# Optimization experiments

Hardware: AMD Instinct MI355X
Metric: run time of the kernel (lower is better)

Reference implementation:

```python
import jax, jax.numpy as jnp
import numpy as np

N_EMBD = 2048
N_HEAD = 8          # config.n_head // 2
HEAD_DIM = 256      # n_embd // (n_head // 2)
HALF = HEAD_DIM // 2
LAMBDA_INIT = 0.8
RMS_EPS = 1.1920929e-07  # torch float32 finfo eps (F.rms_norm default)


def _rms_norm(x):
    # F.rms_norm with no weight: x / sqrt(mean(x^2) + eps)
    return x * jax.lax.rsqrt(jnp.mean(x * x, axis=-1, keepdims=True) + RMS_EPS)


def setup_inputs() -> dict:
    key = jax.random.key(0)
    ks = jax.random.split(key, 10)
    B, T, C = 2, 2048, N_EMBD
    x = jax.random.normal(ks[0], (B, T, C), dtype=jnp.float32)
    wq = jax.random.normal(ks[1], (C, C), dtype=jnp.float32) * 0.02
    wk = jax.random.normal(ks[2], (C, C), dtype=jnp.float32) * 0.02
    wv = jax.random.normal(ks[3], (C, C), dtype=jnp.float32) * 0.02
    wo = jax.random.normal(ks[4], (C, C), dtype=jnp.float32) * 0.02
    lq1 = jax.random.normal(ks[5], (HEAD_DIM,), dtype=jnp.float32) * 0.1
    lk1 = jax.random.normal(ks[6], (HEAD_DIM,), dtype=jnp.float32) * 0.1
    lq2 = jax.random.normal(ks[7], (HEAD_DIM,), dtype=jnp.float32) * 0.1
    lk2 = jax.random.normal(ks[8], (HEAD_DIM,), dtype=jnp.float32) * 0.1
    return {"x": x, "wq": wq, "wk": wk, "wv": wv, "wo": wo,
            "lq1": lq1, "lk1": lk1, "lq2": lq2, "lk2": lk2}


def _causal_attn(q, k, v, mask):
    # q,k: [B,H,T,half], v: [B,H,T,HEAD_DIM]
    scale = 1.0 / jnp.sqrt(jnp.asarray(q.shape[-1], q.dtype))
    scores = jnp.einsum('bhqd,bhkd->bhqk', q, k) * scale
    scores = jnp.where(mask, scores, -jnp.inf)
    attn = jax.nn.softmax(scores, axis=-1)
    return jnp.einsum('bhqk,bhkd->bhqd', attn, v)


def reference(x, wq, wk, wv, wo, lq1, lk1, lq2, lk2):
    B, T, C = x.shape
    lambda_1 = jnp.exp(jnp.sum(lq1 * lk1))
    lambda_2 = jnp.exp(jnp.sum(lq2 * lk2))
    lambda_full = lambda_1 - lambda_2 + LAMBDA_INIT

    q = (x @ wq.T).reshape(B, T, N_HEAD, 2, HALF).transpose(0, 2, 1, 3, 4)  # [B,H,T,2,half]
    k = (x @ wk.T).reshape(B, T, N_HEAD, 2, HALF).transpose(0, 2, 1, 3, 4)
    v = (x @ wv.T).reshape(B, T, N_HEAD, HEAD_DIM).transpose(0, 2, 1, 3)    # [B,H,T,hd]

    q1 = _rms_norm(q[..., 0, :]); q2 = _rms_norm(q[..., 1, :])
    k1 = _rms_norm(k[..., 0, :]); k2 = _rms_norm(k[..., 1, :])

    mask = jnp.tril(jnp.ones((T, T), dtype=bool))
    y1 = _causal_attn(q1, k1, v, mask)
    y2 = _causal_attn(q2, k2, v, mask)
    y = y1 - lambda_full * y2                                               # [B,H,T,hd]

    y = y.transpose(0, 2, 1, 3).reshape(B, T, C)
    return (y @ wo.T) * (1.0 - LAMBDA_INIT)
```

## Files before the change

### kernel.cpp

```cpp
#include <hip/hip_runtime.h>
#include <stdint.h>


typedef __bf16 bf16;
typedef bf16 bf16x8 __attribute__((ext_vector_type(8)));
typedef bf16 bf16x4 __attribute__((ext_vector_type(4)));
typedef bf16 bf16x2 __attribute__((ext_vector_type(2)));
typedef float f32x4 __attribute__((ext_vector_type(4)));

typedef void __attribute__((address_space(1)))* gas_t;
typedef void __attribute__((address_space(3)))* las_t;

__device__ __forceinline__ void gload16(const void* g, void* l) {
  __builtin_amdgcn_global_load_lds((gas_t)(uintptr_t)g, (las_t)(uint32_t)(uintptr_t)l, 16, 0, 0);
}

__device__ __forceinline__ f32x4 mfma16x16(bf16x8 a, bf16x8 b, f32x4 c) {
  return __builtin_amdgcn_mfma_f32_16x16x32_bf16(a, b, c, 0, 0, 0);
}

__global__ __launch_bounds__(256) void cast_f32_bf16(const float* __restrict__ in,
                                                     bf16* __restrict__ out, int n4) {
  int i = blockIdx.x * 256 + threadIdx.x;
  if (i >= n4) return;
  float4 v = ((const float4*)in)[i];
  bf16x4 o;
  o[0] = (bf16)v.x; o[1] = (bf16)v.y; o[2] = (bf16)v.z; o[3] = (bf16)v.w;
  ((bf16x4*)out)[i] = o;
}

__global__ __launch_bounds__(256) void cast4_w(const float* __restrict__ a, const float* __restrict__ b,
                                               const float* __restrict__ c, const float* __restrict__ d,
                                               bf16* __restrict__ oa, bf16* __restrict__ ob,
                                               bf16* __restrict__ oc, bf16* __restrict__ od) {
  int w = blockIdx.y;
  const float* in = (w == 0) ? a : (w == 1) ? b : (w == 2) ? c : d;
  bf16* out = (w == 0) ? oa : (w == 1) ? ob : (w == 2) ? oc : od;
  int i = blockIdx.x * 256 + threadIdx.x;
  float4 v = ((const float4*)in)[i];
  bf16x4 o;
  o[0] = (bf16)v.x; o[1] = (bf16)v.y; o[2] = (bf16)v.z; o[3] = (bf16)v.w;
  ((bf16x4*)out)[i] = o;
}

__global__ void lambda_kernel(const float* __restrict__ lq1, const float* __restrict__ lk1,
                              const float* __restrict__ lq2, const float* __restrict__ lk2,
                              float* __restrict__ out) {
  __shared__ float red[8];
  int tid = threadIdx.x;
  float a = lq1[tid] * lk1[tid];
  float b = lq2[tid] * lk2[tid];
#pragma unroll
  for (int m = 32; m >= 1; m >>= 1) {
    a += __shfl_xor(a, m, 64);
    b += __shfl_xor(b, m, 64);
  }
  if ((tid & 63) == 0) { red[tid >> 6] = a; red[4 + (tid >> 6)] = b; }
  __syncthreads();
  if (tid == 0) {
    float s1 = red[0] + red[1] + red[2] + red[3];
    float s2 = red[4] + red[5] + red[6] + red[7];
    out[0] = expf(s1) - expf(s2) + 0.8f;
  }
}

__global__ __launch_bounds__(512, 2) void gemm_qkv8(const bf16* __restrict__ A,
                                                    const bf16* __restrict__ Bq,
                                                    const bf16* __restrict__ Bk,
                                                    const bf16* __restrict__ Bv,
                                                    bf16* __restrict__ Cq, bf16* __restrict__ Ck,
                                                    bf16* __restrict__ Cv) {
  __shared__ char lds[98304];
  const int K = 2048, nt = 64;

  int p = blockIdx.y * gridDim.x + blockIdx.x;
  int lid = (p & 7) * 48 + (p >> 3);
  const int bm = (lid / 24) * 256;
  const int bnG = (lid % 24) * 256;
  const int z = bnG >> 11;
  const int bn = bnG & 2047;
  const bf16* B = (z == 0) ? Bq : ((z == 1) ? Bk : Bv);

  const int tid = threadIdx.x;
  const int wid = tid >> 6, lane = tid & 63;
  const int l15 = lane & 15, lhi = lane >> 4;
  const int wm = wid >> 2, wn = wid & 3;

  const bf16* aS0 = A + (size_t)(bm + wid * 16 + l15) * K + lhi * 8;
  const bf16* bS0 = B + (size_t)(bn + wid * 16 + l15) * K + lhi * 8;

  auto stA = [&](int t, int pb) {
    char* d = lds + pb * 32768 + wid * 1024;
    const bf16* s = aS0 + t * 32;
    gload16(s, d);
    gload16(s + (size_t)128 * K, d + 8192);
  };
  auto stB = [&](int t, int pb) {
    char* d = lds + pb * 32768 + 16384 + wid * 1024;
    const bf16* s = bS0 + t * 32;
    gload16(s, d);
    gload16(s + (size_t)128 * K, d + 8192);
  };

  const f32x4 fz = {0.f, 0.f, 0.f, 0.f};
  f32x4 acc[8][4];
#pragma unroll
  for (int m = 0; m < 8; ++m)
#pragma unroll
    for (int n = 0; n < 4; ++n) acc[m][n] = fz;

  stA(0, 0); stB(0, 0);
  stA(1, 1); stB(1, 1);
  asm volatile("s_waitcnt vmcnt(4)" ::: "memory");
  __builtin_amdgcn_s_barrier();

  int cur = 0;
  for (int t = 0; t < nt; ++t) {
    const char* ab = lds + cur * 32768;
    const char* bb = ab + 16384;
    int nx2 = cur + 2; if (nx2 >= 3) nx2 -= 3;
    bf16x8 a[8], b0, b1;

#pragma unroll
    for (int m = 0; m < 8; ++m) a[m] = *(const bf16x8*)(ab + (wm * 8 + m) * 1024 + lane * 16);
    b0 = *(const bf16x8*)(bb + (wn * 4 + 0) * 1024 + lane * 16);
    b1 = *(const bf16x8*)(bb + (wn * 4 + 1) * 1024 + lane * 16);
    if (t + 2 < nt) stA(t + 2, nx2);
    __builtin_amdgcn_s_barrier();
    __builtin_amdgcn_s_setprio(1);
#pragma unroll
    for (int m = 0; m < 8; ++m) {
      acc[m][0] = mfma16x16(a[m], b0, acc[m][0]);
      acc[m][1] = mfma16x16(a[m], b1, acc[m][1]);
    }
    __builtin_amdgcn_s_setprio(0);
    __builtin_amdgcn_s_barrier();

    b0 = *(const bf16x8*)(bb + (wn * 4 + 2) * 1024 + lane * 16);
    b1 = *(const bf16x8*)(bb + (wn * 4 + 3) * 1024 + lane * 16);
    if (t + 2 < nt) stB(t + 2, nx2);
    __builtin_amdgcn_s_barrier();
    __builtin_amdgcn_s_setprio(1);
#pragma unroll
    for (int m = 0; m < 8; ++m) {
      acc[m][2] = mfma16x16(a[m], b0, acc[m][2]);
      acc[m][3] = mfma16x16(a[m], b1, acc[m][3]);
    }
    __builtin_amdgcn_s_setprio(0);
    if (t + 2 < nt) {
      asm volatile("s_waitcnt vmcnt(4)" ::: "memory");
    } else {
      asm volatile("s_waitcnt vmcnt(0)" ::: "memory");
    }
    __builtin_amdgcn_s_barrier();

    cur = (cur == 2) ? 0 : cur + 1;
  }

  if (z == 2) {
#pragma unroll
    for (int m = 0; m < 8; ++m)
#pragma unroll
      for (int n = 0; n < 4; ++n)
#pragma unroll
        for (int r = 0; r < 4; ++r) {
          int row = bm + wm * 128 + m * 16 + lhi * 4 + r;
          int col = bn + wn * 64 + n * 16 + l15;
          int bb3 = row >> 11, tt = row & 2047;
          Cv[(size_t)bb3 * 2048 * 2048 + (size_t)col * 2048 + tt] = (bf16)acc[m][n][r];
        }
    return;
  }
  float* ldsf = (float*)lds;
#pragma unroll
  for (int m = 0; m < 8; ++m)
#pragma unroll
    for (int r = 0; r < 4; ++r) {
      float s = acc[m][0][r] * acc[m][0][r] + acc[m][1][r] * acc[m][1][r] +
                acc[m][2][r] * acc[m][2][r] + acc[m][3][r] * acc[m][3][r];
      s += __shfl_xor(s, 1, 64);
      s += __shfl_xor(s, 2, 64);
      s += __shfl_xor(s, 4, 64);
      s += __shfl_xor(s, 8, 64);
      if (l15 == 0) ldsf[(wm * 128 + m * 16 + lhi * 4 + r) * 4 + wn] = s;
    }
  __syncthreads();
  const float osc = (z == 0) ? 0.08838834764831845f : 1.0f;
  bf16* C = (z == 0) ? Cq : Ck;
#pragma unroll
  for (int m = 0; m < 8; ++m) {
#pragma unroll
    for (int r = 0; r < 4; ++r) {
      int rl = wm * 128 + m * 16 + lhi * 4 + r;
      float tot = ldsf[rl * 4 + (wn & 2)] + ldsf[rl * 4 + (wn & 2) + 1];
      float sc = rsqrtf(tot * (1.0f / 128.0f) + 1.1920929e-07f) * osc;
#pragma unroll
      for (int n = 0; n < 4; ++n) {
        int col = bn + wn * 64 + n * 16 + l15;
        C[(size_t)(bm + rl) * 2048 + col] = (bf16)(acc[m][n][r] * sc);
      }
    }
  }
}

__global__ __launch_bounds__(256, 2) void gemm_out(const bf16* __restrict__ A, const bf16* __restrict__ B,
                                                   float* __restrict__ Cf) {
  __shared__ char lds[73728];
  const int K = 2048, nt = 64;

  int p = blockIdx.y * gridDim.x + blockIdx.x;
  int lid = (p & 7) * 32 + (p >> 3);
  const int bm = (lid / 16) * 256;
  const int bn = (lid % 16) * 128;

  const int tid = threadIdx.x;
  const int wid = tid >> 6, lane = tid & 63;
  const int l15 = lane & 15, lhi = lane >> 4;
  const int wm = wid >> 1, wn = wid & 1;

  const bf16* aB = A + (size_t)(bm + l15) * K + lhi * 8;
  const bf16* bB = B + (size_t)(bn + l15) * K + lhi * 8;

  auto stage = [&](int t, int pb) {
    char* base = lds + pb * 24576;
    const int k0 = t * 32;
    gload16(aB + (size_t)((0 + wid) * 16) * K + k0, base + wid * 1024);
    gload16(aB + (size_t)((4 + wid) * 16) * K + k0, base + 4096 + wid * 1024);
    gload16(aB + (size_t)((8 + wid) * 16) * K + k0, base + 8192 + wid * 1024);
    gload16(aB + (size_t)((12 + wid) * 16) * K + k0, base + 12288 + wid * 1024);
    gload16(bB + (size_t)((0 + wid) * 16) * K + k0, base + 16384 + wid * 1024);
    gload16(bB + (size_t)((4 + wid) * 16) * K + k0, base + 20480 + wid * 1024);
  };

  const f32x4 fz = {0.f, 0.f, 0.f, 0.f};
  f32x4 acc[8][4];
#pragma unroll
  for (int m = 0; m < 8; ++m)
#pragma unroll
    for (int n = 0; n < 4; ++n) acc[m][n] = fz;

  stage(0, 0);
  stage(1, 1);
  asm volatile("s_waitcnt vmcnt(6)" ::: "memory");
  __builtin_amdgcn_s_barrier();

  for (int t = 0; t < nt; ++t) {
    const char* ab = lds + (t % 3) * 24576;
    if (t + 2 < nt) stage(t + 2, (t + 2) % 3);
    bf16x8 a[8], b[4];
#pragma unroll
    for (int m = 0; m < 8; ++m)
      a[m] = *(const bf16x8*)(ab + (wm * 8 + m) * 1024 + lane * 16);
#pragma unroll
    for (int n = 0; n < 4; ++n)
      b[n] = *(const bf16x8*)(ab + 16384 + (wn * 4 + n) * 1024 + lane * 16);
    __builtin_amdgcn_s_setprio(1);
#pragma unroll
    for (int m = 0; m < 8; ++m)
#pragma unroll
      for (int n = 0; n < 4; ++n) acc[m][n] = mfma16x16(a[m], b[n], acc[m][n]);
    __builtin_amdgcn_s_setprio(0);
    if (t + 2 < nt) {
      asm volatile("s_waitcnt vmcnt(6)" ::: "memory");
    } else {
      asm volatile("s_waitcnt vmcnt(0)" ::: "memory");
    }
    __builtin_amdgcn_s_barrier();
  }

#pragma unroll
  for (int m = 0; m < 8; ++m)
#pragma unroll
    for (int n = 0; n < 4; ++n)
#pragma unroll
      for (int r = 0; r < 4; ++r) {
        int row = bm + wm * 128 + m * 16 + lhi * 4 + r;
        int col = bn + wn * 64 + n * 16 + l15;
        Cf[(size_t)row * 2048 + col] = acc[m][n][r] * 0.2f;
      }
}

__global__ __launch_bounds__(256) void attn_kernel(const bf16* __restrict__ qb, const bf16* __restrict__ kb,
                                                   const bf16* __restrict__ vtb, bf16* __restrict__ yb,
                                                   const float* __restrict__ lamp) {
  __shared__ char lds[73728];
  const int tid = threadIdx.x;
  const int wid = tid >> 6, lane = tid & 63;
  const int l15 = lane & 15, lhi = lane >> 4;
  char* p1l = lds + 65536 + wid * 2048;
  char* p2l = p1l + 1024;

  const int p = blockIdx.x;
  const int bh = p & 15;
  const int qt = (p < 256) ? (31 - (p >> 4)) : ((p - 256) >> 4);
  const int b = bh >> 3, h = bh & 7;
  const int qr0 = qt * 64 + wid * 16;
  const float lam = lamp[0];

  const bf16* qrow = qb + (size_t)(b * 2048 + qr0 + l15) * 2048 + h * 256 + lhi * 8;
  bf16x8 q1f[4], q2f[4];
#pragma unroll
  for (int s = 0; s < 4; ++s) {
    q1f[s] = *(const bf16x8*)(qrow + s * 32);
    q2f[s] = *(const bf16x8*)(qrow + 128 + s * 32);
  }

  const f32x4 fz = {0.f, 0.f, 0.f, 0.f};
  f32x4 y1[16], y2[16];
#pragma unroll
  for (int f = 0; f < 16; ++f) { y1[f] = fz; y2[f] = fz; }
  float l1[4] = {0.f, 0.f, 0.f, 0.f}, l2[4] = {0.f, 0.f, 0.f, 0.f};

  const int nkt = 2 * qt + 2;
  const bf16* kbase = kb + (size_t)(b * 2048) * 2048 + h * 256;
  const bf16* vbase = vtb + (size_t)b * 2048 * 2048 + (size_t)(h * 256) * 2048;

  auto stageK = [&](int kt2, int pp) {
    const int t0 = kt2 * 32;
    char* kd = lds + pp * 16384 + wid * 1024;
    const bf16* sp = kbase + (size_t)(t0 + l15) * 2048 + wid * 32 + lhi * 8;
    gload16(sp, kd);
    gload16(sp + 16 * 2048, kd + 4096);
    gload16(sp + 128, kd + 8192);
    gload16(sp + 16 * 2048 + 128, kd + 12288);
  };
  auto stageVT = [&](int kt2, int pp) {
    const int t0 = kt2 * 32;
    char* vd = lds + 32768 + pp * 16384;
    const bf16* vp = vbase + (size_t)(wid * 16 + l15) * 2048 + t0 + lhi * 8;
#pragma unroll
    for (int i = 0; i < 4; ++i)
      gload16(vp + (size_t)i * 64 * 2048, vd + (i * 4 + wid) * 1024);
  };

  stageK(0, 0);
  stageVT(0, 0);
  __syncthreads();

  for (int kt = 0; kt < nkt; ++kt) {
    const int cur = kt & 1;
    const int t0 = kt * 32;
    const bool active = (t0 <= qr0 + 15);
    if (kt + 1 < nkt) {
      stageK(kt + 1, cur ^ 1);
      stageVT(kt + 1, cur ^ 1);
    }
    if (active) {
      const char* kc = lds + cur * 16384;
      const char* vc = lds + 32768 + cur * 16384;
      f32x4 s1g[2], s2g[2];
      __builtin_amdgcn_s_setprio(1);
#pragma unroll
      for (int g = 0; g < 2; ++g) {
        f32x4 a1 = fz, a2 = fz;
#pragma unroll
        for (int s = 0; s < 4; ++s) {
          a1 = mfma16x16(q1f[s], *(const bf16x8*)(kc + ((g * 4 + s) * 64 + lane) * 16), a1);
          a2 = mfma16x16(q2f[s], *(const bf16x8*)(kc + 8192 + ((g * 4 + s) * 64 + lane) * 16), a2);
        }
        s1g[g] = a1;
        s2g[g] = a2;
      }
      __builtin_amdgcn_s_setprio(0);
      if (t0 + 31 > qr0) {
#pragma unroll
        for (int g = 0; g < 2; ++g) {
          int col = t0 + g * 16 + l15;
#pragma unroll
          for (int r = 0; r < 4; ++r) {
            int row = qr0 + lhi * 4 + r;
            if (col > row) { s1g[g][r] = -1e30f; s2g[g][r] = -1e30f; }
          }
        }
      }
#pragma unroll
      for (int g = 0; g < 2; ++g) {
#pragma unroll
        for (int r = 0; r < 4; ++r) {
          float p1 = __expf(s1g[g][r] - 12.0f);
          float p2 = __expf(s2g[g][r] - 12.0f);
          l1[r] += p1;
          l2[r] += p2;
          int off = ((lhi * 4 + r) * 32 + g * 16 + l15) * 2;
          *(bf16*)(p1l + off) = (bf16)p1;
          *(bf16*)(p2l + off) = (bf16)p2;
        }
      }
      bf16x8 pa1 = *(const bf16x8*)(p1l + (l15 * 32 + lhi * 8) * 2);
      bf16x8 pa2 = *(const bf16x8*)(p2l + (l15 * 32 + lhi * 8) * 2);
      __builtin_amdgcn_s_setprio(1);
#pragma unroll
      for (int f = 0; f < 16; ++f) {
        bf16x8 vf = *(const bf16x8*)(vc + (f * 64 + lane) * 16);
        y1[f] = mfma16x16(pa1, vf, y1[f]);
        y2[f] = mfma16x16(pa2, vf, y2[f]);
      }
      __builtin_amdgcn_s_setprio(0);
    }
    __syncthreads();
  }

#pragma unroll
  for (int r = 0; r < 4; ++r) {
    float s1 = l1[r], s2 = l2[r];
#pragma unroll
    for (int m = 1; m <= 8; m <<= 1) {
      s1 += __shfl_xor(s1, m, 64);
      s2 += __shfl_xor(s2, m, 64);
    }
    float inv1 = 1.f / s1;
    float inv2 = lam / s2;
    int row = qr0 + lhi * 4 + r;
    bf16* orow = yb + (size_t)(b * 2048 + row) * 2048 + h * 256 + l15;
#pragma unroll
    for (int f = 0; f < 16; ++f) {
      float v = y1[f][r] * inv1 - y2[f][r] * inv2;
      orow[f * 16] = (bf16)v;
    }
  }
}

extern "C" void kernel_launch(void* const* d_in, const int* in_sizes, int n_in,
                              void* d_out, int out_size, void* d_ws, size_t ws_size,
                              hipStream_t stream) {
  const float* x = (const float*)d_in[0];
  const float* wq = (const float*)d_in[1];
  const float* wk = (const float*)d_in[2];
  const float* wv = (const float*)d_in[3];
  const float* wo = (const float*)d_in[4];
  const float* lq1 = (const float*)d_in[5];
  const float* lk1 = (const float*)d_in[6];
  const float* lq2 = (const float*)d_in[7];
  const float* lk2 = (const float*)d_in[8];
  float* out = (float*)d_out;
  char* ws = (char*)d_ws;

  if (ws_size < 117440516) return;

  bf16* xb = (bf16*)(ws + 0);
  bf16* wqb = (bf16*)(ws + 16777216);
  bf16* wkb = (bf16*)(ws + 25165824);
  bf16* wvb = (bf16*)(ws + 33554432);
  bf16* wob = (bf16*)(ws + 41943040);
  bf16* qbuf = (bf16*)(ws + 50331648);
  bf16* kbuf = (bf16*)(ws + 67108864);
  bf16* vtb = (bf16*)(ws + 83886080);
  bf16* ybuf = (bf16*)(ws + 100663296);
  float* lam = (float*)(ws + 117440512);

  cast_f32_bf16<<<8192, 256, 0, stream>>>(x, xb, 2097152);
  cast4_w<<<dim3(4096, 4), 256, 0, stream>>>(wq, wk, wv, wo, wqb, wkb, wvb, wob);
  lambda_kernel<<<1, 256, 0, stream>>>(lq1, lk1, lq2, lk2, lam);

  gemm_qkv8<<<dim3(24, 16), 512, 0, stream>>>(xb, wqb, wkb, wvb, qbuf, kbuf, vtb);

  attn_kernel<<<512, 256, 0, stream>>>(qbuf, kbuf, vtb, ybuf, lam);

  gemm_out<<<dim3(8, 32), 256, 0, stream>>>(ybuf, wob, out);
}
```

Before: 346.6 us.

## Repartition attention waves by softmax branch and widen output GEMM blocks

```diff
diff --git a/kernel.cpp b/kernel.cpp
--- a/kernel.cpp
+++ b/kernel.cpp
@@ -203,65 +203,62 @@
   }
 }
 
-__global__ __launch_bounds__(256, 2) void gemm_out(const bf16* __restrict__ A, const bf16* __restrict__ B,
-                                                   float* __restrict__ Cf) {
+__global__ __launch_bounds__(512) void gemm_out(const bf16* __restrict__ A, const bf16* __restrict__ B,
+                                                float* __restrict__ Cf) {
   __shared__ char lds[73728];
   const int K = 2048, nt = 64;
 
-  int p = blockIdx.y * gridDim.x + blockIdx.x;
+  int p = blockIdx.x;
   int lid = (p & 7) * 32 + (p >> 3);
-  const int bm = (lid / 16) * 256;
-  const int bn = (lid % 16) * 128;
+  const int bm = (lid >> 4) * 256;
+  const int bn = (lid & 15) * 128;
 
   const int tid = threadIdx.x;
   const int wid = tid >> 6, lane = tid & 63;
   const int l15 = lane & 15, lhi = lane >> 4;
   const int wm = wid >> 1, wn = wid & 1;
 
-  const bf16* aB = A + (size_t)(bm + l15) * K + lhi * 8;
-  const bf16* bB = B + (size_t)(bn + l15) * K + lhi * 8;
+  const bf16* aB = A + (size_t)(bm + wid * 16 + l15) * K + lhi * 8;
+  const bf16* bB = B + (size_t)(bn + wid * 16 + l15) * K + lhi * 8;
 
   auto stage = [&](int t, int pb) {
     char* base = lds + pb * 24576;
     const int k0 = t * 32;
-    gload16(aB + (size_t)((0 + wid) * 16) * K + k0, base + wid * 1024);
-    gload16(aB + (size_t)((4 + wid) * 16) * K + k0, base + 4096 + wid * 1024);
-    gload16(aB + (size_t)((8 + wid) * 16) * K + k0, base + 8192 + wid * 1024);
-    gload16(aB + (size_t)((12 + wid) * 16) * K + k0, base + 12288 + wid * 1024);
-    gload16(bB + (size_t)((0 + wid) * 16) * K + k0, base + 16384 + wid * 1024);
-    gload16(bB + (size_t)((4 + wid) * 16) * K + k0, base + 20480 + wid * 1024);
+    gload16(aB + k0, base + wid * 1024);
+    gload16(aB + (size_t)128 * K + k0, base + 8192 + wid * 1024);
+    gload16(bB + k0, base + 16384 + wid * 1024);
   };
 
   const f32x4 fz = {0.f, 0.f, 0.f, 0.f};
-  f32x4 acc[8][4];
-#pragma unroll
-  for (int m = 0; m < 8; ++m)
+  f32x4 acc[4][4];
+#pragma unroll
+  for (int m = 0; m < 4; ++m)
 #pragma unroll
     for (int n = 0; n < 4; ++n) acc[m][n] = fz;
 
   stage(0, 0);
   stage(1, 1);
-  asm volatile("s_waitcnt vmcnt(6)" ::: "memory");
+  asm volatile("s_waitcnt vmcnt(3)" ::: "memory");
   __builtin_amdgcn_s_barrier();
 
   for (int t = 0; t < nt; ++t) {
     const char* ab = lds + (t % 3) * 24576;
     if (t + 2 < nt) stage(t + 2, (t + 2) % 3);
-    bf16x8 a[8], b[4];
-#pragma unroll
-    for (int m = 0; m < 8; ++m)
-      a[m] = *(const bf16x8*)(ab + (wm * 8 + m) * 1024 + lane * 16);
+    bf16x8 a[4], b[4];
+#pragma unroll
+    for (int m = 0; m < 4; ++m)
+      a[m] = *(const bf16x8*)(ab + (wm * 4 + m) * 1024 + lane * 16);
 #pragma unroll
     for (int n = 0; n < 4; ++n)
       b[n] = *(const bf16x8*)(ab + 16384 + (wn * 4 + n) * 1024 + lane * 16);
     __builtin_amdgcn_s_setprio(1);
 #pragma unroll
-    for (int m = 0; m < 8; ++m)
+    for (int m = 0; m < 4; ++m)
 #pragma unroll
       for (int n = 0; n < 4; ++n) acc[m][n] = mfma16x16(a[m], b[n], acc[m][n]);
     __builtin_amdgcn_s_setprio(0);
     if (t + 2 < nt) {
-      asm volatile("s_waitcnt vmcnt(6)" ::: "memory");
+      asm volatile("s_waitcnt vmcnt(3)" ::: "memory");
     } else {
       asm volatile("s_waitcnt vmcnt(0)" ::: "memory");
     }
@@ -269,12 +266,12 @@
   }
 
 #pragma unroll
-  for (int m = 0; m < 8; ++m)
+  for (int m = 0; m < 4; ++m)
 #pragma unroll
     for (int n = 0; n < 4; ++n)
 #pragma unroll
       for (int r = 0; r < 4; ++r) {
-        int row = bm + wm * 128 + m * 16 + lhi * 4 + r;
+        int row = bm + wm * 64 + m * 16 + lhi * 4 + r;
         int col = bn + wn * 64 + n * 16 + l15;
         Cf[(size_t)row * 2048 + col] = acc[m][n][r] * 0.2f;
       }
@@ -287,29 +284,32 @@
   const int tid = threadIdx.x;
   const int wid = tid >> 6, lane = tid & 63;
   const int l15 = lane & 15, lhi = lane >> 4;
-  char* p1l = lds + 65536 + wid * 2048;
-  char* p2l = p1l + 1024;
+  char* pl = lds + 65536 + wid * 2048;
+  const int s = wid >> 1;
+  const int rg = wid & 1;
 
   const int p = blockIdx.x;
   const int bh = p & 15;
   const int qt = (p < 256) ? (31 - (p >> 4)) : ((p - 256) >> 4);
   const int b = bh >> 3, h = bh & 7;
-  const int qr0 = qt * 64 + wid * 16;
+  const int wr0 = qt * 64 + rg * 32;
   const float lam = lamp[0];
 
-  const bf16* qrow = qb + (size_t)(b * 2048 + qr0 + l15) * 2048 + h * 256 + lhi * 8;
-  bf16x8 q1f[4], q2f[4];
-#pragma unroll
-  for (int s = 0; s < 4; ++s) {
-    q1f[s] = *(const bf16x8*)(qrow + s * 32);
-    q2f[s] = *(const bf16x8*)(qrow + 128 + s * 32);
+  bf16x8 qf[2][4];
+#pragma unroll
+  for (int rf = 0; rf < 2; ++rf) {
+    const bf16* qrow = qb + (size_t)(b * 2048 + wr0 + rf * 16 + l15) * 2048 + h * 256 + s * 128 + lhi * 8;
+#pragma unroll
+    for (int c = 0; c < 4; ++c) qf[rf][c] = *(const bf16x8*)(qrow + c * 32);
   }
 
   const f32x4 fz = {0.f, 0.f, 0.f, 0.f};
-  f32x4 y1[16], y2[16];
-#pragma unroll
-  for (int f = 0; f < 16; ++f) { y1[f] = fz; y2[f] = fz; }
-  float l1[4] = {0.f, 0.f, 0.f, 0.f}, l2[4] = {0.f, 0.f, 0.f, 0.f};
+  f32x4 y[2][16];
+#pragma unroll
+  for (int rf = 0; rf < 2; ++rf)
+#pragma unroll
+    for (int f = 0; f < 16; ++f) y[rf][f] = fz;
+  float lsum[2][4] = {{0.f, 0.f, 0.f, 0.f}, {0.f, 0.f, 0.f, 0.f}};
 
   const int nkt = 2 * qt + 2;
   const bf16* kbase = kb + (size_t)(b * 2048) * 2048 + h * 256;
@@ -340,83 +340,102 @@
   for (int kt = 0; kt < nkt; ++kt) {
     const int cur = kt & 1;
     const int t0 = kt * 32;
-    const bool active = (t0 <= qr0 + 15);
+    const bool active = (t0 <= wr0 + 31);
     if (kt + 1 < nkt) {
       stageK(kt + 1, cur ^ 1);
       stageVT(kt + 1, cur ^ 1);
     }
     if (active) {
-      const char* kc = lds + cur * 16384;
+      const char* kc = lds + cur * 16384 + s * 8192;
       const char* vc = lds + 32768 + cur * 16384;
-      f32x4 s1g[2], s2g[2];
+      f32x4 sg[2][2];
       __builtin_amdgcn_s_setprio(1);
 #pragma unroll
-      for (int g = 0; g < 2; ++g) {
-        f32x4 a1 = fz, a2 = fz;
-#pragma unroll
-        for (int s = 0; s < 4; ++s) {
-          a1 = mfma16x16(q1f[s], *(const bf16x8*)(kc + ((g * 4 + s) * 64 + lane) * 16), a1);
-          a2 = mfma16x16(q2f[s], *(const bf16x8*)(kc + 8192 + ((g * 4 + s) * 64 + lane) * 16), a2);
+      for (int rf = 0; rf < 2; ++rf)
+#pragma unroll
+        for (int g = 0; g < 2; ++g) {
+          f32x4 a = fz;
+#pragma unroll
+          for (int ks = 0; ks < 4; ++ks)
+            a = mfma16x16(qf[rf][ks], *(const bf16x8*)(kc + ((g * 4 + ks) * 64 + lane) * 16), a);
+          sg[rf][g] = a;
         }
-        s1g[g] = a1;
-        s2g[g] = a2;
+      __builtin_amdgcn_s_setprio(0);
+      if (t0 + 31 > wr0) {
+#pragma unroll
+        for (int rf = 0; rf < 2; ++rf)
+#pragma unroll
+          for (int g = 0; g < 2; ++g) {
+            int col = t0 + g * 16 + l15;
+#pragma unroll
+            for (int r = 0; r < 4; ++r) {
+              int row = wr0 + rf * 16 + lhi * 4 + r;
+              if (col > row) sg[rf][g][r] = -1e30f;
+            }
+          }
+      }
+#pragma unroll
+      for (int rf = 0; rf < 2; ++rf)
+#pragma unroll
+        for (int g = 0; g < 2; ++g)
+#pragma unroll
+          for (int r = 0; r < 4; ++r) {
+            float pv = __expf(sg[rf][g][r] - 12.0f);
+            lsum[rf][r] += pv;
+            *(bf16*)(pl + rf * 1024 + ((lhi * 4 + r) * 32 + g * 16 + l15) * 2) = (bf16)pv;
+          }
+      bf16x8 pa0 = *(const bf16x8*)(pl + (l15 * 32 + lhi * 8) * 2);
+      bf16x8 pa1 = *(const bf16x8*)(pl + 1024 + (l15 * 32 + lhi * 8) * 2);
+      __builtin_amdgcn_s_setprio(1);
+#pragma unroll
+      for (int f = 0; f < 16; ++f) {
+        bf16x8 vf = *(const bf16x8*)(vc + (f * 64 + lane) * 16);
+        y[0][f] = mfma16x16(pa0, vf, y[0][f]);
+        y[1][f] = mfma16x16(pa1, vf, y[1][f]);
       }
       __builtin_amdgcn_s_setprio(0);
-      if (t0 + 31 > qr0) {
-#pragma unroll
-        for (int g = 0; g < 2; ++g) {
-          int col = t0 + g * 16 + l15;
-#pragma unroll
-          for (int r = 0; r < 4; ++r) {
-            int row = qr0 + lhi * 4 + r;
-            if (col > row) { s1g[g][r] = -1e30f; s2g[g][r] = -1e30f; }
-          }
+    }
+    __syncthreads();
+  }
+
+  float inv[2][4];
+#pragma unroll
+  for (int rf = 0; rf < 2; ++rf)
+#pragma unroll
+    for (int r = 0; r < 4; ++r) {
+      float sv = lsum[rf][r];
+      sv += __shfl_xor(sv, 1, 64);
+      sv += __shfl_xor(sv, 2, 64);
+      sv += __shfl_xor(sv, 4, 64);
+      sv += __shfl_xor(sv, 8, 64);
+      inv[rf][r] = (s == 0) ? (1.f / sv) : (lam / sv);
+    }
+  float* yx = (float*)lds;
+  if (s == 0) {
+#pragma unroll
+    for (int rf = 0; rf < 2; ++rf)
+#pragma unroll
+      for (int f = 0; f < 16; ++f)
+#pragma unroll
+        for (int r = 0; r < 4; ++r) {
+          int rl = rg * 32 + rf * 16 + lhi * 4 + r;
+          yx[rl * 256 + f * 16 + l15] = y[rf][f][r] * inv[rf][r];
+        }
+  }
+  __syncthreads();
+  if (s == 1) {
+#pragma unroll
+    for (int rf = 0; rf < 2; ++rf)
+#pragma unroll
+      for (int r = 0; r < 4; ++r) {
+        int rl = rg * 32 + rf * 16 + lhi * 4 + r;
+        bf16* orow = yb + (size_t)(b * 2048 + qt * 64 + rl) * 2048 + h * 256 + l15;
+#pragma unroll
+        for (int f = 0; f < 16; ++f) {
+          float v = yx[rl * 256 + f * 16 + l15] - y[rf][f][r] * inv[rf][r];
+          orow[f * 16] = (bf16)v;
         }
       }
-#pragma unroll
-      for (int g = 0; g < 2; ++g) {
-#pragma unroll
-        for (int r = 0; r < 4; ++r) {
-          float p1 = __expf(s1g[g][r] - 12.0f);
-          float p2 = __expf(s2g[g][r] - 12.0f);
-          l1[r] += p1;
-          l2[r] += p2;
-          int off = ((lhi * 4 + r) * 32 + g * 16 + l15) * 2;
-          *(bf16*)(p1l + off) = (bf16)p1;
-          *(bf16*)(p2l + off) = (bf16)p2;
-        }
-      }
-      bf16x8 pa1 = *(const bf16x8*)(p1l + (l15 * 32 + lhi * 8) * 2);
-      bf16x8 pa2 = *(const bf16x8*)(p2l + (l15 * 32 + lhi * 8) * 2);
-      __builtin_amdgcn_s_setprio(1);
-#pragma unroll
-      for (int f = 0; f < 16; ++f) {
-        bf16x8 vf = *(const bf16x8*)(vc + (f * 64 + lane) * 16);
-        y1[f] = mfma16x16(pa1, vf, y1[f]);
-        y2[f] = mfma16x16(pa2, vf, y2[f]);
-      }
-      __builtin_amdgcn_s_setprio(0);
-    }
-    __syncthreads();
-  }
-
-#pragma unroll
-  for (int r = 0; r < 4; ++r) {
-    float s1 = l1[r], s2 = l2[r];
-#pragma unroll
-    for (int m = 1; m <= 8; m <<= 1) {
-      s1 += __shfl_xor(s1, m, 64);
-      s2 += __shfl_xor(s2, m, 64);
-    }
-    float inv1 = 1.f / s1;
-    float inv2 = lam / s2;
-    int row = qr0 + lhi * 4 + r;
-    bf16* orow = yb + (size_t)(b * 2048 + row) * 2048 + h * 256 + l15;
-#pragma unroll
-    for (int f = 0; f < 16; ++f) {
-      float v = y1[f][r] * inv1 - y2[f][r] * inv2;
-      orow[f * 16] = (bf16)v;
-    }
   }
 }
 
@@ -456,5 +475,5 @@
 
   attn_kernel<<<512, 256, 0, stream>>>(qbuf, kbuf, vtb, ybuf, lam);
 
-  gemm_out<<<dim3(8, 32), 256, 0, stream>>>(ybuf, wob, out);
-}
+  gemm_out<<<256, 512, 0, stream>>>(ybuf, wob, out);
+}
```

Result: no change. 343.2 us (-1.0%).
